# Optimization experiments

Measured on AMD Instinct MI355X. Metric: run time of the kernel, lower is better.

The kernel has to match this reference:

```python
import jax, jax.numpy as jnp
import numpy as np

B = 256
# (Cin, Cout, K, Hout) for each of the 6 deformable conv layers; input is 33x33
_LAYERS = [(1, 16, 3, 31), (16, 32, 3, 29), (32, 16, 5, 25), (16, 16, 7, 19), (16, 8, 5, 15), (8, 4, 3, 13)]


def setup_inputs() -> dict:
    key = jax.random.key(0)
    ks = jax.random.split(key, 24)
    inp = {"x": jax.random.normal(ks[0], (B, 1, 33, 33), dtype=jnp.float32)}
    for i, (ci, co, k, ho) in enumerate(_LAYERS):
        inp[f"off{i+1}"] = jax.random.normal(ks[1 + i], (1, 2 * k * k, ho, ho), dtype=jnp.float32)
        inp[f"w{i+1}"] = jax.random.normal(ks[7 + i], (co, ci, k, k), dtype=jnp.float32) / float(np.sqrt(ci * k * k))
        inp[f"b{i+1}"] = jnp.zeros((co,), jnp.float32)
    inp["w7"] = jax.random.normal(ks[13], (13 * 13 * 4, 256), dtype=jnp.float32) / 26.0
    inp["b7"] = jnp.zeros((256,), jnp.float32)
    inp["w8"] = jax.random.normal(ks[14], (256, 10), dtype=jnp.float32) / 16.0
    inp["b8"] = jnp.zeros((10,), jnp.float32)
    inp["perm"] = jnp.arange(13 * 13, dtype=jnp.int32)  # fixed spatial permutation (perm_6.ordenar)
    return inp


def _deform_conv(x, offset, weight, bias):
    # torchvision DeformConv2d, stride=1, padding=0, fixed offsets shared across batch.
    Bn, Cin, H, W = x.shape
    Cout, _, K, _ = weight.shape
    Ho, Wo = offset.shape[-2], offset.shape[-1]
    K2 = K * K
    off = offset[0].reshape(K2, 2, Ho, Wo)  # channel layout: [2k]=dy, [2k+1]=dx
    ky, kx = jnp.meshgrid(jnp.arange(K), jnp.arange(K), indexing='ij')
    py = jnp.arange(Ho, dtype=x.dtype)[None, :, None] + ky.reshape(-1, 1, 1) + off[:, 0]  # [K2,Ho,Wo]
    px = jnp.arange(Wo, dtype=x.dtype)[None, None, :] + kx.reshape(-1, 1, 1) + off[:, 1]
    y0f = jnp.floor(py); x0f = jnp.floor(px)
    wy = py - y0f; wx = px - x0f
    y0 = y0f.astype(jnp.int32); x0 = x0f.astype(jnp.int32)
    xf = x.reshape(Bn, Cin, H * W)

    def gather(yi, xi):
        valid = ((yi >= 0) & (yi < H) & (xi >= 0) & (xi < W)).astype(x.dtype)
        idx = (jnp.clip(yi, 0, H - 1) * W + jnp.clip(xi, 0, W - 1)).reshape(-1)
        v = xf[:, :, idx].reshape(Bn, Cin, K2, Ho, Wo)
        return v * valid[None, None]

    s = (gather(y0, x0) * ((1 - wy) * (1 - wx))[None, None]
         + gather(y0, x0 + 1) * ((1 - wy) * wx)[None, None]
         + gather(y0 + 1, x0) * (wy * (1 - wx))[None, None]
         + gather(y0 + 1, x0 + 1) * (wy * wx)[None, None])  # [B,Cin,K2,Ho,Wo]
    out = jnp.einsum('bckhw,ock->bohw', s, weight.reshape(Cout, Cin, K2))
    return out + bias[None, :, None, None]


def reference(x, off1, off2, off3, off4, off5, off6,
              w1, b1, w2, b2, w3, b3, w4, b4, w5, b5, w6, b6,
              w7, b7, w8, b8, perm):
    offs = (off1, off2, off3, off4, off5, off6)
    ws = (w1, w2, w3, w4, w5, w6)
    bs = (b1, b2, b3, b4, b5, b6)
    for off, w, b in zip(offs, ws, bs):
        x = jax.nn.relu(_deform_conv(x, off, w, b))
    Bn = x.shape[0]
    x = x.reshape(Bn, 4, 13 * 13)[:, :, perm].reshape(Bn, -1)  # perm_6.ordenar as spatial permutation
    h = jax.nn.relu(x @ w7 + b7)
    return h @ w8 + b8
```

## Files before the change

### kernel.cpp

```cpp
#include <hip/hip_runtime.h>

struct WtArgs { const float* src[6]; int co[6], ci[6], k2[6], dstoff[6]; };

__global__ __launch_bounds__(256)
void transpose_weights(WtArgs a, float* __restrict__ dst0)
{
    const int L = blockIdx.x;
    const float* __restrict__ s = a.src[L];
    float* __restrict__ d = dst0 + a.dstoff[L];
    const int co = a.co[L], ci = a.ci[L], k2 = a.k2[L];
    const int n = co * ci * k2;
    for (int i = threadIdx.x; i < n; i += 256) {
        int k = i % k2;
        int c = (i / k2) % ci;
        int o = i / (k2 * ci);
        d[(k * ci + c) * co + o] = s[i];
    }
}

template<int CIN, int CINW, int COUT, int K, int H, int W, int HO, int WO,
         int S, int KSEG, int NT, bool COMB, bool SPLITOUT>
__global__ __launch_bounds__(NT)
void deform_lds(const float* __restrict__ x0, const float* __restrict__ x1,
                const float* __restrict__ off, const float* __restrict__ wT,
                const float* __restrict__ bias, float* __restrict__ y,
                size_t pstride)
{
    constexpr int K2 = K * K, HW = H * W, P = HO * WO;
    constexpr int PW = ((P + 63) / 64) * 64;
    constexpr int KLEN = (K2 + KSEG - 1) / KSEG;
    constexpr int PSTR = (COUT % 2 == 0) ? COUT + 1 : COUT;
    static_assert(NT >= KSEG * PW, "NT too small for KSEG*PW");

    __shared__ __align__(16) float simg[HW * S];
    __shared__ float part[(KSEG > 1) ? (KSEG - 1) * P * PSTR : 1];

    const int tid = threadIdx.x;
    const int b   = blockIdx.x;
    const int h   = SPLITOUT ? blockIdx.y : 0;

    const size_t xoff = (size_t)b * CINW * HW + (SPLITOUT ? (size_t)h * CIN * HW : 0);
    const float* xb  = x0 + xoff;
    const float* xb1 = COMB ? (x1 + xoff) : nullptr;
    for (int i = tid; i < CIN * HW; i += NT) {
        int c = i / HW, hw = i - c * HW;
        float v;
        if constexpr (COMB) v = fmaxf(xb[i] + xb1[i], 0.f);
        else                v = xb[i];
        simg[hw * S + c] = v;
    }
    __syncthreads();

    const int g  = tid / PW;
    const int p  = tid - g * PW;
    const int pc = (p < P) ? p : (P - 1);
    const bool active = (p < P);

    float acc[COUT];
#pragma unroll
    for (int o = 0; o < COUT; ++o) acc[o] = 0.f;

    if (g < KSEG) {
        if (g == 0 && (!SPLITOUT || h == 0)) {
#pragma unroll
            for (int o = 0; o < COUT; ++o) acc[o] = bias[o];
        }
        const int ho = pc / WO, wo = pc - ho * WO;
        const int kb = g * KLEN;

        const int kf = (kb < K2) ? kb : (K2 - 1);
        float ndy = off[(2 * kf)     * P + pc];
        float ndx = off[(2 * kf + 1) * P + pc];

#pragma unroll 1
        for (int j = 0; j < KLEN; ++j) {
            const int k  = kb + j;
            const int kk = (k < K2) ? k : (K2 - 1);
            const float dy = ndy, dx = ndx;
            const int kn = (k + 1 < K2) ? (k + 1) : (K2 - 1);
            ndy = off[(2 * kn)     * P + pc];
            ndx = off[(2 * kn + 1) * P + pc];

            const int ky = kk / K, kx = kk - ky * K;
            const float py = (float)(ho + ky) + dy;
            const float px = (float)(wo + kx) + dx;
            const float y0f = floorf(py), x0f = floorf(px);
            const float wy = py - y0f, wx = px - x0f;
            const int y0 = (int)y0f, x0 = (int)x0f;
            const int y1 = y0 + 1,  x1i = x0 + 1;
            const bool vy0 = ((unsigned)y0  < (unsigned)H);
            const bool vy1 = ((unsigned)y1  < (unsigned)H);
            const bool vx0 = ((unsigned)x0  < (unsigned)W);
            const bool vx1 = ((unsigned)x1i < (unsigned)W);
            const int cy0 = min(max(y0, 0), H - 1) * W;
            const int cy1 = min(max(y1, 0), H - 1) * W;
            const int cx0 = min(max(x0, 0), W - 1);
            const int cx1 = min(max(x1i, 0), W - 1);
            float w00 = (vy0 && vx0) ? (1.f - wy) * (1.f - wx) : 0.f;
            float w01 = (vy0 && vx1) ? (1.f - wy) * wx         : 0.f;
            float w10 = (vy1 && vx0) ? wy * (1.f - wx)         : 0.f;
            float w11 = (vy1 && vx1) ? wy * wx                 : 0.f;
            if constexpr (K2 % KSEG != 0) {
                const float kv = (k < K2) ? 1.f : 0.f;
                w00 *= kv; w01 *= kv; w10 *= kv; w11 *= kv;
            }

            const float* __restrict__ r00 = simg + (cy0 + cx0) * S;
            const float* __restrict__ r01 = simg + (cy0 + cx1) * S;
            const float* __restrict__ r10 = simg + (cy1 + cx0) * S;
            const float* __restrict__ r11 = simg + (cy1 + cx1) * S;
            const int kku = __builtin_amdgcn_readfirstlane(kk);
            const float* __restrict__ wk = wT + kku * (CINW * COUT)
                                         + (SPLITOUT ? h * (CIN * COUT) : 0);

            if constexpr (CIN % 4 == 0) {
#pragma unroll
                for (int c4 = 0; c4 < CIN / 4; ++c4) {
                    const float4 v00 = *(const float4*)(r00 + c4 * 4);
                    const float4 v01 = *(const float4*)(r01 + c4 * 4);
                    const float4 v10 = *(const float4*)(r10 + c4 * 4);
                    const float4 v11 = *(const float4*)(r11 + c4 * 4);
                    float4 sa;
                    sa.x = fmaf(w00, v00.x, fmaf(w01, v01.x, fmaf(w10, v10.x, w11 * v11.x)));
                    sa.y = fmaf(w00, v00.y, fmaf(w01, v01.y, fmaf(w10, v10.y, w11 * v11.y)));
                    sa.z = fmaf(w00, v00.z, fmaf(w01, v01.z, fmaf(w10, v10.z, w11 * v11.z)));
                    sa.w = fmaf(w00, v00.w, fmaf(w01, v01.w, fmaf(w10, v10.w, w11 * v11.w)));
                    const float* __restrict__ wc = wk + (c4 * 4) * COUT;
#pragma unroll
                    for (int o = 0; o < COUT; ++o) acc[o] = fmaf(wc[o], sa.x, acc[o]);
#pragma unroll
                    for (int o = 0; o < COUT; ++o) acc[o] = fmaf(wc[COUT + o], sa.y, acc[o]);
#pragma unroll
                    for (int o = 0; o < COUT; ++o) acc[o] = fmaf(wc[2 * COUT + o], sa.z, acc[o]);
#pragma unroll
                    for (int o = 0; o < COUT; ++o) acc[o] = fmaf(wc[3 * COUT + o], sa.w, acc[o]);
                }
            } else {
#pragma unroll
                for (int c = 0; c < CIN; ++c) {
                    float sa = fmaf(w00, r00[c], fmaf(w01, r01[c],
                               fmaf(w10, r10[c], w11 * r11[c])));
#pragma unroll
                    for (int o = 0; o < COUT; ++o)
                        acc[o] = fmaf(wk[c * COUT + o], sa, acc[o]);
                }
            }
        }

        if (g > 0 && active) {
#pragma unroll
            for (int o = 0; o < COUT; ++o)
                part[(g - 1) * (P * PSTR) + p * PSTR + o] = acc[o];
        }
    }

    if constexpr (KSEG > 1) __syncthreads();

    if (g == 0 && active) {
        if constexpr (KSEG > 1) {
#pragma unroll
            for (int gg = 1; gg < KSEG; ++gg)
#pragma unroll
                for (int o = 0; o < COUT; ++o)
                    acc[o] += part[(gg - 1) * (P * PSTR) + p * PSTR + o];
        }
        float* yb = y + (SPLITOUT ? (size_t)h * pstride : 0) + (size_t)b * COUT * P;
#pragma unroll
        for (int o = 0; o < COUT; ++o)
            yb[o * P + p] = SPLITOUT ? acc[o] : fmaxf(acc[o], 0.f);
    }
}

__global__ __launch_bounds__(256)
void fc_head(const float* __restrict__ x6, const float* __restrict__ w7,
             const float* __restrict__ b7, const float* __restrict__ w8,
             const float* __restrict__ b8, const int* __restrict__ perm,
             float* __restrict__ out)
{
    constexpr int BPB = 4;
    constexpr int F   = 676;
    __shared__ float sx[BPB][F];
    __shared__ float sh[BPB][256];

    const int tid = threadIdx.x;
    const int b0  = blockIdx.x * BPB;

    for (int i = tid; i < BPB * F; i += 256) {
        int bb = i / F, f = i - bb * F;
        int c = f / 169, p = f - c * 169;
        sx[bb][f] = x6[(size_t)(b0 + bb) * F + c * 169 + perm[p]];
    }
    __syncthreads();

    float acc[BPB];
#pragma unroll
    for (int bb = 0; bb < BPB; ++bb) acc[bb] = b7[tid];
#pragma unroll 4
    for (int i = 0; i < F; ++i) {
        const float wv = w7[i * 256 + tid];
#pragma unroll
        for (int bb = 0; bb < BPB; ++bb)
            acc[bb] = fmaf(sx[bb][i], wv, acc[bb]);
    }
#pragma unroll
    for (int bb = 0; bb < BPB; ++bb) sh[bb][tid] = fmaxf(acc[bb], 0.f);
    __syncthreads();

    if (tid < BPB * 10) {
        int bb = tid / 10, t = tid - bb * 10;
        float a = b8[t];
#pragma unroll 8
        for (int j = 0; j < 256; ++j)
            a = fmaf(sh[bb][j], w8[j * 10 + t], a);
        out[(size_t)(b0 + bb) * 10 + t] = a;
    }
}

extern "C" void kernel_launch(void* const* d_in, const int* in_sizes, int n_in,
                              void* d_out, int out_size, void* d_ws, size_t ws_size,
                              hipStream_t stream)
{
    const float* x    = (const float*)d_in[0];
    const float* off1 = (const float*)d_in[1];
    const float* w1   = (const float*)d_in[2];
    const float* b1   = (const float*)d_in[3];
    const float* off2 = (const float*)d_in[4];
    const float* w2   = (const float*)d_in[5];
    const float* b2   = (const float*)d_in[6];
    const float* off3 = (const float*)d_in[7];
    const float* w3   = (const float*)d_in[8];
    const float* b3   = (const float*)d_in[9];
    const float* off4 = (const float*)d_in[10];
    const float* w4   = (const float*)d_in[11];
    const float* b4   = (const float*)d_in[12];
    const float* off5 = (const float*)d_in[13];
    const float* w5   = (const float*)d_in[14];
    const float* b5   = (const float*)d_in[15];
    const float* off6 = (const float*)d_in[16];
    const float* w6   = (const float*)d_in[17];
    const float* b6   = (const float*)d_in[18];
    const float* w7   = (const float*)d_in[19];
    const float* b7   = (const float*)d_in[20];
    const float* w8   = (const float*)d_in[21];
    const float* b8   = (const float*)d_in[22];
    const int*   perm = (const int*)d_in[23];
    float* out = (float*)d_out;

    const int woff[6] = {0, 144, 4752, 17552, 30096, 33296};
    float* ws   = (float*)d_ws;
    float* wt   = ws;
    float* buf0 = ws + 33792;
    float* buf1 = buf0 + 3936256;

    float* a1   = buf0;
    float* a2   = buf1;
    float* a3   = buf0;
    float* p1L3 = ws + 10859520;
    float* a4p0 = buf1;
    float* a4p1 = buf1 + 1478656;
    float* a5   = buf0;
    float* a6   = buf1;

    const bool splitL3 = (ws_size >= (size_t)(10859520 + 2560000) * sizeof(float));
    const size_t pstrL3 = (size_t)(p1L3 - a3);
    const size_t pstrL4 = 1478656;

    WtArgs wa;
    wa.src[0] = w1; wa.src[1] = w2; wa.src[2] = w3;
    wa.src[3] = w4; wa.src[4] = w5; wa.src[5] = w6;
    const int cos[6] = {16, 32, 16, 16, 8, 4};
    const int cis[6] = {1, 16, 32, 16, 16, 8};
    const int k2s[6] = {9, 9, 25, 49, 25, 9};
    for (int i = 0; i < 6; ++i) {
        wa.co[i] = cos[i]; wa.ci[i] = cis[i];
        wa.k2[i] = k2s[i]; wa.dstoff[i] = woff[i];
    }
    transpose_weights<<<dim3(6), dim3(256), 0, stream>>>(wa, wt);

    const dim3 g1(256), g2(256, 2);
    deform_lds< 1,  1, 16, 3, 33, 33, 31, 31,  1, 1, 1024, false, false>
        <<<g1, dim3(1024), 0, stream>>>(x,  nullptr, off1, wt + woff[0], b1, a1, 0);
    deform_lds<16, 16, 32, 3, 31, 31, 29, 29, 20, 1, 1024, false, false>
        <<<g1, dim3(1024), 0, stream>>>(a1, nullptr, off2, wt + woff[1], b2, a2, 0);

    if (splitL3) {
        deform_lds<16, 32, 16, 5, 29, 29, 25, 25, 20, 1, 1024, false, true>
            <<<g2, dim3(1024), 0, stream>>>(a2, nullptr, off3, wt + woff[2], b3, a3, pstrL3);
        deform_lds< 8, 16, 16, 7, 25, 25, 19, 19, 12, 2,  768, true,  true>
            <<<g2, dim3(768),  0, stream>>>(a3, p1L3,   off4, wt + woff[3], b4, a4p0, pstrL4);
    } else {
        deform_lds<32, 32, 16, 5, 29, 29, 25, 25, 36, 1, 1024, false, false>
            <<<g1, dim3(1024), 0, stream>>>(a2, nullptr, off3, wt + woff[2], b3, a3, 0);
        deform_lds< 8, 16, 16, 7, 25, 25, 19, 19, 12, 2,  768, false, true>
            <<<g2, dim3(768),  0, stream>>>(a3, nullptr, off4, wt + woff[3], b4, a4p0, pstrL4);
    }

    deform_lds<16, 16,  8, 5, 19, 19, 15, 15, 20, 4, 1024, true,  false>
        <<<g1, dim3(1024), 0, stream>>>(a4p0, a4p1, off5, wt + woff[4], b5, a5, 0);
    deform_lds< 8,  8,  4, 3, 15, 15, 13, 13, 12, 5,  960, false, false>
        <<<g1, dim3(960),  0, stream>>>(a5, nullptr, off6, wt + woff[5], b6, a6, 0);

    fc_head<<<dim3(64), dim3(256), 0, stream>>>(a6, w7, b7, w8, b8, perm, out);
}
```

Before: 279.8 us.

## Split layer-2 input channels across two blocks and widen FC head grid

Layer 2 now splits its 16 input channels over two blocks per image (grid 256x2), each writing partial sums. Layer 3 then adds and ReLUs the two partials while loading its input. This doubles the block count for layer 2 and shrinks its LDS image, at the cost of extra partial-sum traffic and a larger workspace requirement. The FC head also moves to one image per block (256 blocks instead of 64), which adds parallelism but reads w7 four times as often.

```diff
diff --git a/kernel.cpp b/kernel.cpp
--- a/kernel.cpp
+++ b/kernel.cpp
@@ -19,7 +19,7 @@
 }
 
 template<int CIN, int CINW, int COUT, int K, int H, int W, int HO, int WO,
-         int S, int KSEG, int NT, bool COMB, bool SPLITOUT>
+         int S, int KSEG, int NT, int NCOMB, bool SPLITOUT>
 __global__ __launch_bounds__(NT)
 void deform_lds(const float* __restrict__ x0, const float* __restrict__ x1,
                 const float* __restrict__ off, const float* __restrict__ wT,
@@ -41,12 +41,12 @@
 
     const size_t xoff = (size_t)b * CINW * HW + (SPLITOUT ? (size_t)h * CIN * HW : 0);
     const float* xb  = x0 + xoff;
-    const float* xb1 = COMB ? (x1 + xoff) : nullptr;
+    const float* xb1 = (NCOMB == 2) ? (x1 + xoff) : nullptr;
     for (int i = tid; i < CIN * HW; i += NT) {
         int c = i / HW, hw = i - c * HW;
         float v;
-        if constexpr (COMB) v = fmaxf(xb[i] + xb1[i], 0.f);
-        else                v = xb[i];
+        if constexpr (NCOMB == 2) v = fmaxf(xb[i] + xb1[i], 0.f);
+        else                      v = xb[i];
         simg[hw * S + c] = v;
     }
     __syncthreads();
@@ -177,42 +177,32 @@
              const float* __restrict__ b8, const int* __restrict__ perm,
              float* __restrict__ out)
 {
-    constexpr int BPB = 4;
-    constexpr int F   = 676;
-    __shared__ float sx[BPB][F];
-    __shared__ float sh[BPB][256];
+    constexpr int F = 676;
+    __shared__ float sx[F];
+    __shared__ float sh[256];
 
     const int tid = threadIdx.x;
-    const int b0  = blockIdx.x * BPB;
-
-    for (int i = tid; i < BPB * F; i += 256) {
-        int bb = i / F, f = i - bb * F;
-        int c = f / 169, p = f - c * 169;
-        sx[bb][f] = x6[(size_t)(b0 + bb) * F + c * 169 + perm[p]];
+    const int b   = blockIdx.x;
+
+    for (int i = tid; i < F; i += 256) {
+        int c = i / 169, p = i - c * 169;
+        sx[i] = x6[(size_t)b * F + c * 169 + perm[p]];
     }
     __syncthreads();
 
-    float acc[BPB];
-#pragma unroll
-    for (int bb = 0; bb < BPB; ++bb) acc[bb] = b7[tid];
+    float acc = b7[tid];
 #pragma unroll 4
-    for (int i = 0; i < F; ++i) {
-        const float wv = w7[i * 256 + tid];
-#pragma unroll
-        for (int bb = 0; bb < BPB; ++bb)
-            acc[bb] = fmaf(sx[bb][i], wv, acc[bb]);
-    }
-#pragma unroll
-    for (int bb = 0; bb < BPB; ++bb) sh[bb][tid] = fmaxf(acc[bb], 0.f);
+    for (int i = 0; i < F; ++i)
+        acc = fmaf(sx[i], w7[i * 256 + tid], acc);
+    sh[tid] = fmaxf(acc, 0.f);
     __syncthreads();
 
-    if (tid < BPB * 10) {
-        int bb = tid / 10, t = tid - bb * 10;
-        float a = b8[t];
+    if (tid < 10) {
+        float a = b8[tid];
 #pragma unroll 8
         for (int j = 0; j < 256; ++j)
-            a = fmaf(sh[bb][j], w8[j * 10 + t], a);
-        out[(size_t)(b0 + bb) * 10 + t] = a;
+            a = fmaf(sh[j], w8[j * 10 + tid], a);
+        out[(size_t)b * 10 + tid] = a;
     }
 }
 
@@ -254,6 +244,7 @@
 
     float* a1   = buf0;
     float* a2   = buf1;
+    float* p1L2 = ws + 13419520;
     float* a3   = buf0;
     float* p1L3 = ws + 10859520;
     float* a4p0 = buf1;
@@ -261,8 +252,10 @@
     float* a5   = buf0;
     float* a6   = buf1;
 
-    const bool splitL3 = (ws_size >= (size_t)(10859520 + 2560000) * sizeof(float));
+    const bool splitL3 = (ws_size >= (size_t)13419520 * sizeof(float));
+    const bool splitL2 = (ws_size >= (size_t)20308992 * sizeof(float));
     const size_t pstrL3 = (size_t)(p1L3 - a3);
+    const size_t pstrL2 = (size_t)(p1L2 - a2);
     const size_t pstrL4 = 1478656;
 
     WtArgs wa;
@@ -278,27 +271,38 @@
     transpose_weights<<<dim3(6), dim3(256), 0, stream>>>(wa, wt);
 
     const dim3 g1(256), g2(256, 2);
-    deform_lds< 1,  1, 16, 3, 33, 33, 31, 31,  1, 1, 1024, false, false>
+    deform_lds< 1,  1, 16, 3, 33, 33, 31, 31,  1, 1, 1024, 1, false>
         <<<g1, dim3(1024), 0, stream>>>(x,  nullptr, off1, wt + woff[0], b1, a1, 0);
-    deform_lds<16, 16, 32, 3, 31, 31, 29, 29, 20, 1, 1024, false, false>
-        <<<g1, dim3(1024), 0, stream>>>(a1, nullptr, off2, wt + woff[1], b2, a2, 0);
+
+    if (splitL2) {
+        deform_lds< 8, 16, 32, 3, 31, 31, 29, 29, 12, 1, 1024, 1, true>
+            <<<g2, dim3(1024), 0, stream>>>(a1, nullptr, off2, wt + woff[1], b2, a2, pstrL2);
+    } else {
+        deform_lds<16, 16, 32, 3, 31, 31, 29, 29, 20, 1, 1024, 1, false>
+            <<<g1, dim3(1024), 0, stream>>>(a1, nullptr, off2, wt + woff[1], b2, a2, 0);
+    }
 
     if (splitL3) {
-        deform_lds<16, 32, 16, 5, 29, 29, 25, 25, 20, 1, 1024, false, true>
-            <<<g2, dim3(1024), 0, stream>>>(a2, nullptr, off3, wt + woff[2], b3, a3, pstrL3);
-        deform_lds< 8, 16, 16, 7, 25, 25, 19, 19, 12, 2,  768, true,  true>
-            <<<g2, dim3(768),  0, stream>>>(a3, p1L3,   off4, wt + woff[3], b4, a4p0, pstrL4);
+        if (splitL2) {
+            deform_lds<16, 32, 16, 5, 29, 29, 25, 25, 20, 1, 1024, 2, true>
+                <<<g2, dim3(1024), 0, stream>>>(a2, p1L2, off3, wt + woff[2], b3, a3, pstrL3);
+        } else {
+            deform_lds<16, 32, 16, 5, 29, 29, 25, 25, 20, 1, 1024, 1, true>
+                <<<g2, dim3(1024), 0, stream>>>(a2, nullptr, off3, wt + woff[2], b3, a3, pstrL3);
+        }
+        deform_lds< 8, 16, 16, 7, 25, 25, 19, 19, 12, 2,  768, 2, true>
+            <<<g2, dim3(768),  0, stream>>>(a3, p1L3, off4, wt + woff[3], b4, a4p0, pstrL4);
     } else {
-        deform_lds<32, 32, 16, 5, 29, 29, 25, 25, 36, 1, 1024, false, false>
+        deform_lds<32, 32, 16, 5, 29, 29, 25, 25, 36, 1, 1024, 1, false>
             <<<g1, dim3(1024), 0, stream>>>(a2, nullptr, off3, wt + woff[2], b3, a3, 0);
-        deform_lds< 8, 16, 16, 7, 25, 25, 19, 19, 12, 2,  768, false, true>
+        deform_lds< 8, 16, 16, 7, 25, 25, 19, 19, 12, 2,  768, 1, true>
             <<<g2, dim3(768),  0, stream>>>(a3, nullptr, off4, wt + woff[3], b4, a4p0, pstrL4);
     }
 
-    deform_lds<16, 16,  8, 5, 19, 19, 15, 15, 20, 4, 1024, true,  false>
+    deform_lds<16, 16,  8, 5, 19, 19, 15, 15, 20, 4, 1024, 2, false>
         <<<g1, dim3(1024), 0, stream>>>(a4p0, a4p1, off5, wt + woff[4], b5, a5, 0);
-    deform_lds< 8,  8,  4, 3, 15, 15, 13, 13, 12, 5,  960, false, false>
+    deform_lds< 8,  8,  4, 3, 15, 15, 13, 13, 12, 5,  960, 1, false>
         <<<g1, dim3(960),  0, stream>>>(a5, nullptr, off6, wt + woff[5], b6, a6, 0);
 
-    fc_head<<<dim3(64), dim3(256), 0, stream>>>(a6, w7, b7, w8, b8, perm, out);
+    fc_head<<<dim3(256), dim3(256), 0, stream>>>(a6, w7, b7, w8, b8, perm, out);
 }
```

After: 272.1 us. -2.8%, faster.
